# Kernel optimization log

Hardware: AMD Instinct MI355X
Metric: run time of the kernel (lower is better)

## Reference

```python
import jax, jax.numpy as jnp
import numpy as np

WH, WW = 14, 14
NUM_HEADS = 12
HEAD_DIM = 64
HIDDEN = NUM_HEADS * HEAD_DIM
SEQ = WH * WW + 1  # 197, includes cls token
NUM_REL = (2 * WH - 1) * (2 * WW - 1) + 3  # 732


def _relative_position_index(wh, ww):
    # Static numpy computation, identical to BeitRelativePositionBias buffer
    coords = np.stack(np.meshgrid(np.arange(wh), np.arange(ww), indexing='ij'))  # [2, wh, ww]
    flat = coords.reshape(2, -1)  # [2, wh*ww]
    rel = flat[:, :, None] - flat[:, None, :]  # [2, N, N]
    rel = rel.transpose(1, 2, 0).astype(np.int64)  # [N, N, 2]
    rel[..., 0] += wh - 1
    rel[..., 1] += ww - 1
    rel[..., 0] *= 2 * ww - 1
    nrd = (2 * wh - 1) * (2 * ww - 1) + 3
    idx = np.zeros((wh * ww + 1, wh * ww + 1), dtype=np.int64)
    idx[1:, 1:] = rel.sum(-1)
    idx[0, :] = nrd - 3
    idx[:, 0] = nrd - 2
    idx[0, 0] = nrd - 1
    return idx

_REL_IDX = jnp.asarray(_relative_position_index(WH, WW))  # [SEQ, SEQ]


def setup_inputs() -> dict:
    key = jax.random.key(0)
    ks = jax.random.split(key, 7)
    B = 64
    s = 1.0 / np.sqrt(HIDDEN)
    return {
        'hidden_states': jax.random.normal(ks[0], (B, SEQ, HIDDEN), jnp.float32),
        'Wq': jax.random.normal(ks[1], (HIDDEN, HIDDEN), jnp.float32) * s,
        'bq': jax.random.normal(ks[2], (HIDDEN,), jnp.float32) * 0.02,
        'Wk': jax.random.normal(ks[3], (HIDDEN, HIDDEN), jnp.float32) * s,
        'Wv': jax.random.normal(ks[4], (HIDDEN, HIDDEN), jnp.float32) * s,
        'bv': jax.random.normal(ks[5], (HIDDEN,), jnp.float32) * 0.02,
        'bias_table': jax.random.normal(ks[6], (NUM_REL, NUM_HEADS), jnp.float32) * 0.02,
    }


def reference(hidden_states, Wq, bq, Wk, Wv, bv, bias_table):
    B, S, D = hidden_states.shape
    H, Dh = NUM_HEADS, HEAD_DIM

    def heads(x):  # [B,S,D] -> [B,H,S,Dh]
        return x.reshape(B, S, H, Dh).transpose(0, 2, 1, 3)

    q = heads(hidden_states @ Wq + bq)
    k = heads(hidden_states @ Wk)           # key projection has no bias
    v = heads(hidden_states @ Wv + bv)

    scores = jnp.einsum('bhqd,bhkd->bhqk', q, k) / jnp.sqrt(jnp.float32(Dh))
    # relative position bias: gather [SEQ,SEQ,H] -> [H,SEQ,SEQ]
    rel_bias = bias_table[_REL_IDX].transpose(2, 0, 1)
    scores = scores + rel_bias[None]

    probs = jax.nn.softmax(scores, axis=-1)  # dropout prob = 0 (eval)
    ctx = jnp.einsum('bhqk,bhkd->bhqd', probs, v)
    ctx = ctx.transpose(0, 2, 1, 3).reshape(B, S, D)
    return ctx
```

## Files before the change

kernel.cpp:

```cpp
#include <hip/hip_runtime.h>
#include <hip/hip_bf16.h>
#include <stdint.h>

typedef unsigned short u16;
typedef __attribute__((ext_vector_type(4))) float f32x4;
typedef __attribute__((ext_vector_type(8))) short s16x8;
typedef __attribute__((ext_vector_type(4))) unsigned short u16x4;
typedef __attribute__((ext_vector_type(4))) float fvec4;

#define NH 12
#define DH 64
#define HID 768
#define SEQ 197
#define VP 224
#define NREL 732
#define BATCH 64
#define MROWS (BATCH*SEQ)
#define NCAT (3*HID)
#define BK 64
#define MT 99
#define NT 18
#define NWG (MT*NT)
#define AWG (768*13)
#define QKSTRIDE (SEQ*DH)

static __device__ __forceinline__ u16 f2bf(float f) {
  union { float f; uint32_t u; } v; v.f = f;
  uint32_t u = v.u;
  return (u16)((u + 0x7FFFu + ((u >> 16) & 1u)) >> 16);
}
static __device__ __forceinline__ float bf2f(u16 v) {
  union { uint32_t u; float f; } x; x.u = ((uint32_t)v) << 16; return x.f;
}

__global__ __launch_bounds__(256) void conv_x(const float* __restrict__ x, u16* __restrict__ xb, int n8) {
  int i = blockIdx.x * 256 + threadIdx.x;
  if (i >= n8) return;
  fvec4 a = ((const fvec4*)x)[2 * i];
  fvec4 b = ((const fvec4*)x)[2 * i + 1];
  s16x8 r;
  r[0] = (short)f2bf(a[0]); r[1] = (short)f2bf(a[1]); r[2] = (short)f2bf(a[2]); r[3] = (short)f2bf(a[3]);
  r[4] = (short)f2bf(b[0]); r[5] = (short)f2bf(b[1]); r[6] = (short)f2bf(b[2]); r[7] = (short)f2bf(b[3]);
  ((s16x8*)xb)[i] = r;
}

__global__ __launch_bounds__(256) void conv_w(const float* __restrict__ Wq, const float* __restrict__ Wk,
                                              const float* __restrict__ Wv, u16* __restrict__ Wt) {
  __shared__ float t[64][65];
  int n0 = blockIdx.x * 64;
  int k0 = blockIdx.y * 64;
  int m = n0 / HID;
  const float* W = (m == 0) ? Wq : ((m == 1) ? Wk : Wv);
  int nn0 = n0 - m * HID;
  for (int i = threadIdx.x; i < 64 * 64; i += 256) {
    int r = i >> 6, c = i & 63;
    t[r][c] = W[(size_t)(k0 + r) * HID + nn0 + c];
  }
  __syncthreads();
  for (int i = threadIdx.x; i < 64 * 64; i += 256) {
    int r = i >> 6, c = i & 63;
    Wt[(size_t)(n0 + r) * HID + k0 + c] = f2bf(t[c][r]);
  }
}

__global__ __launch_bounds__(256) void conv_b(const float* __restrict__ bq, const float* __restrict__ bv,
                                              float* __restrict__ bc) {
  int i = blockIdx.x * 256 + threadIdx.x;
  if (i < NCAT) {
    int m = i / HID, r = i - m * HID;
    bc[i] = (m == 0) ? bq[r] : ((m == 2) ? bv[r] : 0.f);
  }
}

__global__ __launch_bounds__(256) void expand_bias(const float* __restrict__ bias_table, u16* __restrict__ Bxt) {
  int i = blockIdx.x * 256 + threadIdx.x;
  if (i >= NH * 208 * 208) return;
  int h = i / (208 * 208);
  int r = i - h * 208 * 208;
  int k = r / 208, q = r - k * 208;
  float v;
  if (k >= SEQ) v = -1e30f;
  else if (q >= SEQ) v = 0.f;
  else {
    int idx;
    if (q == 0) idx = (k == 0) ? 731 : 729;
    else if (k == 0) idx = 730;
    else {
      int iq = (q - 1) / 14, jq = (q - 1) % 14;
      int ik = (k - 1) / 14, jk = (k - 1) % 14;
      idx = (iq - ik + 13) * 27 + (jq - jk + 13);
    }
    v = bias_table[(size_t)idx * NH + h];
  }
  Bxt[i] = f2bf(v);
}


static __device__ __forceinline__ void stage128(const u16* __restrict__ gbase, int grow0, int growmax,
                                                u16* lds, int w, int l) {
#pragma unroll
  for (int i = 0; i < 4; ++i) {
    int ch = w * 4 + i;
    int r = ch * 8 + (l >> 3);
    int grow = grow0 + r; if (grow > growmax) grow = growmax;
    int c = (l & 7) ^ (l >> 3);
    const u16* g = gbase + (size_t)grow * HID + c * 8;
    __builtin_amdgcn_global_load_lds((const __attribute__((address_space(1))) void*)g,
                                     (__attribute__((address_space(3))) void*)(lds + ch * 512),
                                     16, 0, 0);
  }
}

static __device__ __forceinline__ void compute128(const u16* As, const u16* Bs, int wr, int wc,
                                                  int li, int lg, f32x4 acc[4][4]) {
#pragma unroll
  for (int kk = 0; kk < 2; ++kk) {
    s16x8 af[4], bf[4];
#pragma unroll
    for (int mi = 0; mi < 4; ++mi) {
      int r = wr * 64 + mi * 16 + li;
      int c = (kk * 4 + lg) ^ (r & 7);
      af[mi] = *(const s16x8*)((const char*)As + r * 128 + c * 16);
    }
#pragma unroll
    for (int ni = 0; ni < 4; ++ni) {
      int r = wc * 64 + ni * 16 + li;
      int c = (kk * 4 + lg) ^ (r & 7);
      bf[ni] = *(const s16x8*)((const char*)Bs + r * 128 + c * 16);
    }
#pragma unroll
    for (int mi = 0; mi < 4; ++mi)
#pragma unroll
      for (int ni = 0; ni < 4; ++ni)
        acc[mi][ni] = __builtin_amdgcn_mfma_f32_16x16x32_bf16(af[mi], bf[ni], acc[mi][ni], 0, 0, 0);
  }
}

__global__ __launch_bounds__(256, 2) void qkv_gemm(const u16* __restrict__ Xb, const u16* __restrict__ Wt,
                                                   const float* __restrict__ bc, u16* __restrict__ Qw,
                                                   u16* __restrict__ Kw, u16* __restrict__ Vt) {
  __shared__ u16 LDSU[32768];
  u16* As0 = LDSU;
  u16* Bs0 = LDSU + 8192;
  u16* As1 = LDSU + 16384;
  u16* Bs1 = LDSU + 24576;
  const int tid = threadIdx.x;
  const int w = tid >> 6, l = tid & 63;
  const int wr = w >> 1, wc = w & 1;
  const int lg = l >> 4, li = l & 15;

  const int lin = blockIdx.x;
  const int xcd = lin & 7;
  const int pos = lin >> 3;
  const int work = (xcd < 6 ? xcd * 223 : 6 * 223 + (xcd - 6) * 222) + pos;
  const int mt = work / NT, nt = work - mt * NT;
  const int arow0 = mt * 128, brow0 = nt * 128;

  f32x4 acc[4][4] = {};

  stage128(Xb, arow0, MROWS - 1, As0, w, l);
  stage128(Wt, brow0, NCAT - 1, Bs0, w, l);
  __syncthreads();

  for (int kt2 = 0; kt2 < 6; ++kt2) {
    const int kt = kt2 * 2;
    stage128(Xb + (kt + 1) * BK, arow0, MROWS - 1, As1, w, l);
    stage128(Wt + (kt + 1) * BK, brow0, NCAT - 1, Bs1, w, l);
    compute128(As0, Bs0, wr, wc, li, lg, acc);
    __syncthreads();
    if (kt2 < 5) {
      stage128(Xb + (kt + 2) * BK, arow0, MROWS - 1, As0, w, l);
      stage128(Wt + (kt + 2) * BK, brow0, NCAT - 1, Bs0, w, l);
    }
    compute128(As1, Bs1, wr, wc, li, lg, acc);
    __syncthreads();
  }

  const int mblk = nt / 6;
  float bcv[4];
#pragma unroll
  for (int ni = 0; ni < 4; ++ni) bcv[ni] = bc[brow0 + wc * 64 + ni * 16 + li];

  if (mblk < 2) {
    u16* __restrict__ dst = (mblk == 0) ? Qw : Kw;
    const float scale = (mblk == 0) ? 0.125f : 1.0f;
    int hv[4], dv[4];
#pragma unroll
    for (int ni = 0; ni < 4; ++ni) {
      int cloc = brow0 - mblk * HID + wc * 64 + ni * 16 + li;
      hv[ni] = cloc >> 6; dv[ni] = cloc & 63;
    }
#pragma unroll
    for (int mi = 0; mi < 4; ++mi) {
#pragma unroll
      for (int j = 0; j < 4; ++j) {
        int row = arow0 + wr * 64 + mi * 16 + lg * 4 + j;
        if (row < MROWS) {
          int b = row / SEQ, s = row - b * SEQ;
#pragma unroll
          for (int ni = 0; ni < 4; ++ni)
            dst[((size_t)(b * NH + hv[ni]) * SEQ + s) * DH + dv[ni]] = f2bf((acc[mi][ni][j] + bcv[ni]) * scale);
        }
      }
    }
  } else {
#pragma unroll
    for (int mi = 0; mi < 4; ++mi) {
#pragma unroll
      for (int ni = 0; ni < 4; ++ni) {
        u16x4 pk;
#pragma unroll
        for (int j = 0; j < 4; ++j) pk[j] = f2bf(acc[mi][ni][j] + bcv[ni]);
        *(u16x4*)&LDSU[w * 4352 + (ni * 16 + li) * 68 + mi * 16 + lg * 4] = pk;
      }
    }
    __syncthreads();
    const int cw0 = brow0 - 2 * HID;
#pragma unroll 4
    for (int p = 0; p < 64; ++p) {
      int i = p * 256 + tid;
      int r = i & 127, c = i >> 7;
      int wq = ((r >> 6) << 1) | (c >> 6);
      u16 v = LDSU[wq * 4352 + (c & 63) * 68 + (r & 63)];
      int row = arow0 + r;
      if (row < MROWS) {
        int b = row / SEQ, s = row - b * SEQ;
        int cl = cw0 + c;
        int h = cl >> 6, d = cl & 63;
        Vt[((size_t)(b * NH + h) * DH + d) * VP + s] = v;
      }
    }
  }
}

__global__ __launch_bounds__(64, 3) void attn(const u16* __restrict__ Qw, const u16* __restrict__ Kw,
                                              const u16* __restrict__ Vt, const u16* __restrict__ Bxt,
                                              float* __restrict__ out) {
  __shared__ u16 P[16 * 232];
  const int l = threadIdx.x;
  const int lg = l >> 4, li = l & 15;
  const int lin = blockIdx.x;
  const int work = (lin & 7) * (AWG / 8) + (lin >> 3);
  const int bh = work / 13, qf = work - bh * 13;
  const int b = bh / NH, h = bh - b * NH;

  for (int t = l; t < 16 * 24; t += 64) {
    int rr = t / 24, cc = t - rr * 24;
    P[rr * 232 + 208 + cc] = 0;
  }

  const u16* Qb = Qw + (size_t)bh * QKSTRIDE;
  const u16* Kb = Kw + (size_t)bh * QKSTRIDE;
  const u16* Vb = Vt + (size_t)bh * DH * VP;
  const u16* Bhp = Bxt + (size_t)h * 208 * 208 + qf * 16 + lg * 4;

  s16x8 a0 = *(const s16x8*)(Qb + (size_t)(qf * 16 + li) * DH + lg * 8);
  s16x8 a1 = *(const s16x8*)(Qb + (size_t)(qf * 16 + li) * DH + 32 + lg * 8);

  u16x4 bb[13];
#pragma unroll
  for (int kf = 0; kf < 13; ++kf)
    bb[kf] = *(const u16x4*)(Bhp + (size_t)(kf * 16 + li) * 208);

  s16x8 kb0[3], kb1[3];
#pragma unroll
  for (int p = 0; p < 3; ++p) {
    kb0[p] = *(const s16x8*)(Kb + (size_t)(p * 16 + li) * DH + lg * 8);
    kb1[p] = *(const s16x8*)(Kb + (size_t)(p * 16 + li) * DH + 32 + lg * 8);
  }
  f32x4 S[13];
#pragma unroll
  for (int kf = 0; kf < 13; ++kf) {
    const int slot = kf % 3;
    f32x4 c = {};
    c = __builtin_amdgcn_mfma_f32_16x16x32_bf16(a0, kb0[slot], c, 0, 0, 0);
    c = __builtin_amdgcn_mfma_f32_16x16x32_bf16(a1, kb1[slot], c, 0, 0, 0);
    if (kf + 3 < 13) {
      kb0[slot] = *(const s16x8*)(Kb + (size_t)((kf + 3) * 16 + li) * DH + lg * 8);
      kb1[slot] = *(const s16x8*)(Kb + (size_t)((kf + 3) * 16 + li) * DH + 32 + lg * 8);
    }
#pragma unroll
    for (int j = 0; j < 4; ++j)
      S[kf][j] = c[j] + bf2f(bb[kf][j]);
  }

  float rinv[4];
#pragma unroll
  for (int j = 0; j < 4; ++j) {
    float m = S[0][j];
#pragma unroll
    for (int kf = 1; kf < 13; ++kf) m = fmaxf(m, S[kf][j]);
    m = fmaxf(m, __shfl_xor(m, 1));
    m = fmaxf(m, __shfl_xor(m, 2));
    m = fmaxf(m, __shfl_xor(m, 4));
    m = fmaxf(m, __shfl_xor(m, 8));
    float sum = 0.f;
#pragma unroll
    for (int kf = 0; kf < 13; ++kf) {
      float p = __expf(S[kf][j] - m);
      S[kf][j] = p;
      sum += p;
    }
    sum += __shfl_xor(sum, 1);
    sum += __shfl_xor(sum, 2);
    sum += __shfl_xor(sum, 4);
    sum += __shfl_xor(sum, 8);
    rinv[j] = 1.0f / sum;
  }

#pragma unroll
  for (int kf = 0; kf < 13; ++kf)
#pragma unroll
    for (int j = 0; j < 4; ++j)
      P[(lg * 4 + j) * 232 + kf * 16 + li] = f2bf(S[kf][j]);

  s16x8 vb[4];
#pragma unroll
  for (int p = 0; p < 4; ++p)
    vb[p] = *(const s16x8*)(Vb + (size_t)((p / 7) * 16 + li) * VP + (p % 7) * 32 + lg * 8);
  f32x4 o[4];
#pragma unroll
  for (int nf = 0; nf < 4; ++nf) {
    f32x4 c = {};
#pragma unroll
    for (int t = 0; t < 7; ++t) {
      const int u = nf * 7 + t, slot = u & 3;
      s16x8 pa = *(const s16x8*)(&P[li * 232 + t * 32 + lg * 8]);
      c = __builtin_amdgcn_mfma_f32_16x16x32_bf16(pa, vb[slot], c, 0, 0, 0);
      if (u + 4 < 28) {
        const int u2 = u + 4;
        vb[slot] = *(const s16x8*)(Vb + (size_t)((u2 / 7) * 16 + li) * VP + (u2 % 7) * 32 + lg * 8);
      }
    }
    o[nf] = c;
  }
#pragma unroll
  for (int nf = 0; nf < 4; ++nf) {
#pragma unroll
    for (int j = 0; j < 4; ++j) {
      int q = qf * 16 + lg * 4 + j;
      if (q < SEQ)
        out[((size_t)(b * SEQ + q)) * HID + h * DH + nf * 16 + li] = o[nf][j] * rinv[j];
    }
  }
}

extern "C" void kernel_launch(void* const* d_in, const int* in_sizes, int n_in,
                              void* d_out, int out_size, void* d_ws, size_t ws_size,
                              hipStream_t stream) {
  const float* hidden = (const float*)d_in[0];
  const float* Wq = (const float*)d_in[1];
  const float* bq = (const float*)d_in[2];
  const float* Wk = (const float*)d_in[3];
  const float* Wv = (const float*)d_in[4];
  const float* bv = (const float*)d_in[5];
  const float* btab = (const float*)d_in[6];
  float* out = (float*)d_out;

  char* ws = (char*)d_ws;
  u16* Xb  = (u16*)(ws);
  u16* Wt  = (u16*)(ws + 19365888);
  float* bc = (float*)(ws + 22904832);
  u16* Bxt = (u16*)(ws + 22914048);
  u16* Qw  = (u16*)(ws + 23952384);
  u16* Kw  = (u16*)(ws + 43322368);
  u16* Vt  = (u16*)(ws + 62692352);

  conv_x<<<dim3(4728), dim3(256), 0, stream>>>(hidden, Xb, (MROWS * HID) / 8);
  conv_w<<<dim3(NCAT / 64, HID / 64), dim3(256), 0, stream>>>(Wq, Wk, Wv, Wt);
  conv_b<<<dim3(9), dim3(256), 0, stream>>>(bq, bv, bc);
  qkv_gemm<<<dim3(NWG), dim3(256), 0, stream>>>(Xb, Wt, bc, Qw, Kw, Vt);
  expand_bias<<<dim3((NH * 208 * 208 + 255) / 256), dim3(256), 0, stream>>>(btab, Bxt);
  attn<<<dim3(AWG), dim3(64), 0, stream>>>(Qw, Kw, Vt, Bxt, out);
}
```

Before: 141.1 us.

## Merge prep kernels into one launch and process 32 queries per attention wave

The four preprocessing kernels (input cast, weight transpose-cast, bias concat, relative-bias expansion) become one kernel that picks its job from the block index. This removes three launches and their inter-kernel gaps. The attention kernel now has each wave handle two 16-row query tiles. That halves the K and V fragment loads per query and the number of workgroups, at the cost of more registers, so the occupancy hint drops from 3 to 2. The last query tile now reads bias and Q rows past the padded extent; the workspace offsets are shifted slightly, and those rows are never written out.

```diff
diff --git a/kernel.cpp b/kernel.cpp
--- a/kernel.cpp
+++ b/kernel.cpp
@@ -21,8 +21,13 @@
 #define MT 99
 #define NT 18
 #define NWG (MT*NT)
-#define AWG (768*13)
+#define AWG2 (768*7)
 #define QKSTRIDE (SEQ*DH)
+
+#define PB_X 4728
+#define PB_W (PB_X + 432)
+#define PB_B (PB_W + 9)
+#define PB_E (PB_B + 2028)
 
 static __device__ __forceinline__ u16 f2bf(float f) {
   union { float f; uint32_t u; } v; v.f = f;
@@ -33,68 +38,66 @@
   union { uint32_t u; float f; } x; x.u = ((uint32_t)v) << 16; return x.f;
 }
 
-__global__ __launch_bounds__(256) void conv_x(const float* __restrict__ x, u16* __restrict__ xb, int n8) {
-  int i = blockIdx.x * 256 + threadIdx.x;
-  if (i >= n8) return;
-  fvec4 a = ((const fvec4*)x)[2 * i];
-  fvec4 b = ((const fvec4*)x)[2 * i + 1];
-  s16x8 r;
-  r[0] = (short)f2bf(a[0]); r[1] = (short)f2bf(a[1]); r[2] = (short)f2bf(a[2]); r[3] = (short)f2bf(a[3]);
-  r[4] = (short)f2bf(b[0]); r[5] = (short)f2bf(b[1]); r[6] = (short)f2bf(b[2]); r[7] = (short)f2bf(b[3]);
-  ((s16x8*)xb)[i] = r;
-}
-
-__global__ __launch_bounds__(256) void conv_w(const float* __restrict__ Wq, const float* __restrict__ Wk,
-                                              const float* __restrict__ Wv, u16* __restrict__ Wt) {
+__global__ __launch_bounds__(256) void prep_all(const float* __restrict__ x,
+                                                const float* __restrict__ Wq, const float* __restrict__ Wk,
+                                                const float* __restrict__ Wv, const float* __restrict__ bq,
+                                                const float* __restrict__ bv, const float* __restrict__ btab,
+                                                u16* __restrict__ xb, u16* __restrict__ Wt,
+                                                float* __restrict__ bc, u16* __restrict__ Bxt) {
   __shared__ float t[64][65];
-  int n0 = blockIdx.x * 64;
-  int k0 = blockIdx.y * 64;
-  int m = n0 / HID;
-  const float* W = (m == 0) ? Wq : ((m == 1) ? Wk : Wv);
-  int nn0 = n0 - m * HID;
-  for (int i = threadIdx.x; i < 64 * 64; i += 256) {
-    int r = i >> 6, c = i & 63;
-    t[r][c] = W[(size_t)(k0 + r) * HID + nn0 + c];
-  }
-  __syncthreads();
-  for (int i = threadIdx.x; i < 64 * 64; i += 256) {
-    int r = i >> 6, c = i & 63;
-    Wt[(size_t)(n0 + r) * HID + k0 + c] = f2bf(t[c][r]);
-  }
-}
-
-__global__ __launch_bounds__(256) void conv_b(const float* __restrict__ bq, const float* __restrict__ bv,
-                                              float* __restrict__ bc) {
-  int i = blockIdx.x * 256 + threadIdx.x;
-  if (i < NCAT) {
-    int m = i / HID, r = i - m * HID;
-    bc[i] = (m == 0) ? bq[r] : ((m == 2) ? bv[r] : 0.f);
-  }
-}
-
-__global__ __launch_bounds__(256) void expand_bias(const float* __restrict__ bias_table, u16* __restrict__ Bxt) {
-  int i = blockIdx.x * 256 + threadIdx.x;
-  if (i >= NH * 208 * 208) return;
-  int h = i / (208 * 208);
-  int r = i - h * 208 * 208;
-  int k = r / 208, q = r - k * 208;
-  float v;
-  if (k >= SEQ) v = -1e30f;
-  else if (q >= SEQ) v = 0.f;
-  else {
-    int idx;
-    if (q == 0) idx = (k == 0) ? 731 : 729;
-    else if (k == 0) idx = 730;
+  const int bi = blockIdx.x;
+  const int tid = threadIdx.x;
+  if (bi < PB_X) {
+    int i = bi * 256 + tid;
+    fvec4 a = ((const fvec4*)x)[2 * i];
+    fvec4 b = ((const fvec4*)x)[2 * i + 1];
+    s16x8 r;
+    r[0] = (short)f2bf(a[0]); r[1] = (short)f2bf(a[1]); r[2] = (short)f2bf(a[2]); r[3] = (short)f2bf(a[3]);
+    r[4] = (short)f2bf(b[0]); r[5] = (short)f2bf(b[1]); r[6] = (short)f2bf(b[2]); r[7] = (short)f2bf(b[3]);
+    ((s16x8*)xb)[i] = r;
+  } else if (bi < PB_W) {
+    int f = bi - PB_X;
+    int n0 = (f % 36) * 64, k0 = (f / 36) * 64;
+    int m = n0 / HID;
+    const float* W = (m == 0) ? Wq : ((m == 1) ? Wk : Wv);
+    int nn0 = n0 - m * HID;
+    for (int i = tid; i < 64 * 64; i += 256) {
+      int r = i >> 6, c = i & 63;
+      t[r][c] = W[(size_t)(k0 + r) * HID + nn0 + c];
+    }
+    __syncthreads();
+    for (int i = tid; i < 64 * 64; i += 256) {
+      int r = i >> 6, c = i & 63;
+      Wt[(size_t)(n0 + r) * HID + k0 + c] = f2bf(t[c][r]);
+    }
+  } else if (bi < PB_B) {
+    int i = (bi - PB_W) * 256 + tid;
+    if (i < NCAT) {
+      int m = i / HID, r = i - m * HID;
+      bc[i] = (m == 0) ? bq[r] : ((m == 2) ? bv[r] : 0.f);
+    }
+  } else {
+    int i = (bi - PB_B) * 256 + tid;
+    int h = i / (208 * 208);
+    int r = i - h * 208 * 208;
+    int k = r / 208, q = r - k * 208;
+    float v;
+    if (k >= SEQ) v = -1e30f;
+    else if (q >= SEQ) v = 0.f;
     else {
-      int iq = (q - 1) / 14, jq = (q - 1) % 14;
-      int ik = (k - 1) / 14, jk = (k - 1) % 14;
-      idx = (iq - ik + 13) * 27 + (jq - jk + 13);
-    }
-    v = bias_table[(size_t)idx * NH + h];
-  }
-  Bxt[i] = f2bf(v);
-}
-
+      int idx;
+      if (q == 0) idx = (k == 0) ? 731 : 729;
+      else if (k == 0) idx = 730;
+      else {
+        int iq = (q - 1) / 14, jq = (q - 1) % 14;
+        int ik = (k - 1) / 14, jk = (k - 1) % 14;
+        idx = (iq - ik + 13) * 27 + (jq - jk + 13);
+      }
+      v = btab[(size_t)idx * NH + h];
+    }
+    Bxt[i] = f2bf(v);
+  }
+}
 
 static __device__ __forceinline__ void stage128(const u16* __restrict__ gbase, int grow0, int growmax,
                                                 u16* lds, int w, int l) {
@@ -233,34 +236,40 @@
   }
 }
 
-__global__ __launch_bounds__(64, 3) void attn(const u16* __restrict__ Qw, const u16* __restrict__ Kw,
+__global__ __launch_bounds__(64, 2) void attn(const u16* __restrict__ Qw, const u16* __restrict__ Kw,
                                               const u16* __restrict__ Vt, const u16* __restrict__ Bxt,
                                               float* __restrict__ out) {
-  __shared__ u16 P[16 * 232];
+  __shared__ u16 P[2][16 * 232];
   const int l = threadIdx.x;
   const int lg = l >> 4, li = l & 15;
   const int lin = blockIdx.x;
-  const int work = (lin & 7) * (AWG / 8) + (lin >> 3);
-  const int bh = work / 13, qf = work - bh * 13;
+  const int work = (lin & 7) * (AWG2 / 8) + (lin >> 3);
+  const int bh = work / 7, qp = work - bh * 7;
   const int b = bh / NH, h = bh - b * NH;
-
-  for (int t = l; t < 16 * 24; t += 64) {
-    int rr = t / 24, cc = t - rr * 24;
-    P[rr * 232 + 208 + cc] = 0;
+  const int q0 = qp * 32;
+
+  for (int t = l; t < 2 * 16 * 24; t += 64) {
+    int g = t / (16 * 24), r2 = t - g * (16 * 24);
+    int rr = r2 / 24, cc = r2 - rr * 24;
+    P[g][rr * 232 + 208 + cc] = 0;
   }
 
   const u16* Qb = Qw + (size_t)bh * QKSTRIDE;
   const u16* Kb = Kw + (size_t)bh * QKSTRIDE;
   const u16* Vb = Vt + (size_t)bh * DH * VP;
-  const u16* Bhp = Bxt + (size_t)h * 208 * 208 + qf * 16 + lg * 4;
-
-  s16x8 a0 = *(const s16x8*)(Qb + (size_t)(qf * 16 + li) * DH + lg * 8);
-  s16x8 a1 = *(const s16x8*)(Qb + (size_t)(qf * 16 + li) * DH + 32 + lg * 8);
-
-  u16x4 bb[13];
-#pragma unroll
-  for (int kf = 0; kf < 13; ++kf)
-    bb[kf] = *(const u16x4*)(Bhp + (size_t)(kf * 16 + li) * 208);
+  const u16* Bhp = Bxt + (size_t)h * 208 * 208 + q0 + lg * 4;
+
+  s16x8 a0 = *(const s16x8*)(Qb + (size_t)(q0 + li) * DH + lg * 8);
+  s16x8 a1 = *(const s16x8*)(Qb + (size_t)(q0 + li) * DH + 32 + lg * 8);
+  s16x8 a2 = *(const s16x8*)(Qb + (size_t)(q0 + 16 + li) * DH + lg * 8);
+  s16x8 a3 = *(const s16x8*)(Qb + (size_t)(q0 + 16 + li) * DH + 32 + lg * 8);
+
+  u16x4 bb0[13], bb1[13];
+#pragma unroll
+  for (int kf = 0; kf < 13; ++kf) {
+    bb0[kf] = *(const u16x4*)(Bhp + (size_t)(kf * 16 + li) * 208);
+    bb1[kf] = *(const u16x4*)(Bhp + (size_t)(kf * 16 + li) * 208 + 16);
+  }
 
   s16x8 kb0[3], kb1[3];
 #pragma unroll
@@ -268,79 +277,89 @@
     kb0[p] = *(const s16x8*)(Kb + (size_t)(p * 16 + li) * DH + lg * 8);
     kb1[p] = *(const s16x8*)(Kb + (size_t)(p * 16 + li) * DH + 32 + lg * 8);
   }
-  f32x4 S[13];
+  f32x4 S0[13], S1[13];
 #pragma unroll
   for (int kf = 0; kf < 13; ++kf) {
     const int slot = kf % 3;
-    f32x4 c = {};
-    c = __builtin_amdgcn_mfma_f32_16x16x32_bf16(a0, kb0[slot], c, 0, 0, 0);
-    c = __builtin_amdgcn_mfma_f32_16x16x32_bf16(a1, kb1[slot], c, 0, 0, 0);
+    f32x4 c0 = {}, c1 = {};
+    c0 = __builtin_amdgcn_mfma_f32_16x16x32_bf16(a0, kb0[slot], c0, 0, 0, 0);
+    c0 = __builtin_amdgcn_mfma_f32_16x16x32_bf16(a1, kb1[slot], c0, 0, 0, 0);
+    c1 = __builtin_amdgcn_mfma_f32_16x16x32_bf16(a2, kb0[slot], c1, 0, 0, 0);
+    c1 = __builtin_amdgcn_mfma_f32_16x16x32_bf16(a3, kb1[slot], c1, 0, 0, 0);
     if (kf + 3 < 13) {
       kb0[slot] = *(const s16x8*)(Kb + (size_t)((kf + 3) * 16 + li) * DH + lg * 8);
       kb1[slot] = *(const s16x8*)(Kb + (size_t)((kf + 3) * 16 + li) * DH + 32 + lg * 8);
     }
 #pragma unroll
-    for (int j = 0; j < 4; ++j)
-      S[kf][j] = c[j] + bf2f(bb[kf][j]);
-  }
-
-  float rinv[4];
+    for (int j = 0; j < 4; ++j) {
+      S0[kf][j] = c0[j] + bf2f(bb0[kf][j]);
+      S1[kf][j] = c1[j] + bf2f(bb1[kf][j]);
+    }
+  }
+
+  float rinv0[4], rinv1[4];
 #pragma unroll
   for (int j = 0; j < 4; ++j) {
-    float m = S[0][j];
-#pragma unroll
-    for (int kf = 1; kf < 13; ++kf) m = fmaxf(m, S[kf][j]);
-    m = fmaxf(m, __shfl_xor(m, 1));
-    m = fmaxf(m, __shfl_xor(m, 2));
-    m = fmaxf(m, __shfl_xor(m, 4));
-    m = fmaxf(m, __shfl_xor(m, 8));
-    float sum = 0.f;
+    float m0 = S0[0][j], m1 = S1[0][j];
+#pragma unroll
+    for (int kf = 1; kf < 13; ++kf) { m0 = fmaxf(m0, S0[kf][j]); m1 = fmaxf(m1, S1[kf][j]); }
+    m0 = fmaxf(m0, __shfl_xor(m0, 1)); m1 = fmaxf(m1, __shfl_xor(m1, 1));
+    m0 = fmaxf(m0, __shfl_xor(m0, 2)); m1 = fmaxf(m1, __shfl_xor(m1, 2));
+    m0 = fmaxf(m0, __shfl_xor(m0, 4)); m1 = fmaxf(m1, __shfl_xor(m1, 4));
+    m0 = fmaxf(m0, __shfl_xor(m0, 8)); m1 = fmaxf(m1, __shfl_xor(m1, 8));
+    float s0 = 0.f, s1 = 0.f;
 #pragma unroll
     for (int kf = 0; kf < 13; ++kf) {
-      float p = __expf(S[kf][j] - m);
-      S[kf][j] = p;
-      sum += p;
-    }
-    sum += __shfl_xor(sum, 1);
-    sum += __shfl_xor(sum, 2);
-    sum += __shfl_xor(sum, 4);
-    sum += __shfl_xor(sum, 8);
-    rinv[j] = 1.0f / sum;
+      float p0 = __expf(S0[kf][j] - m0); S0[kf][j] = p0; s0 += p0;
+      float p1 = __expf(S1[kf][j] - m1); S1[kf][j] = p1; s1 += p1;
+    }
+    s0 += __shfl_xor(s0, 1); s1 += __shfl_xor(s1, 1);
+    s0 += __shfl_xor(s0, 2); s1 += __shfl_xor(s1, 2);
+    s0 += __shfl_xor(s0, 4); s1 += __shfl_xor(s1, 4);
+    s0 += __shfl_xor(s0, 8); s1 += __shfl_xor(s1, 8);
+    rinv0[j] = 1.0f / s0; rinv1[j] = 1.0f / s1;
   }
 
 #pragma unroll
   for (int kf = 0; kf < 13; ++kf)
 #pragma unroll
-    for (int j = 0; j < 4; ++j)
-      P[(lg * 4 + j) * 232 + kf * 16 + li] = f2bf(S[kf][j]);
+    for (int j = 0; j < 4; ++j) {
+      P[0][(lg * 4 + j) * 232 + kf * 16 + li] = f2bf(S0[kf][j]);
+      P[1][(lg * 4 + j) * 232 + kf * 16 + li] = f2bf(S1[kf][j]);
+    }
 
   s16x8 vb[4];
 #pragma unroll
   for (int p = 0; p < 4; ++p)
     vb[p] = *(const s16x8*)(Vb + (size_t)((p / 7) * 16 + li) * VP + (p % 7) * 32 + lg * 8);
-  f32x4 o[4];
+  f32x4 o0[4], o1[4];
 #pragma unroll
   for (int nf = 0; nf < 4; ++nf) {
-    f32x4 c = {};
+    f32x4 c0 = {}, c1 = {};
 #pragma unroll
     for (int t = 0; t < 7; ++t) {
       const int u = nf * 7 + t, slot = u & 3;
-      s16x8 pa = *(const s16x8*)(&P[li * 232 + t * 32 + lg * 8]);
-      c = __builtin_amdgcn_mfma_f32_16x16x32_bf16(pa, vb[slot], c, 0, 0, 0);
+      s16x8 pa0 = *(const s16x8*)(&P[0][li * 232 + t * 32 + lg * 8]);
+      s16x8 pa1 = *(const s16x8*)(&P[1][li * 232 + t * 32 + lg * 8]);
+      c0 = __builtin_amdgcn_mfma_f32_16x16x32_bf16(pa0, vb[slot], c0, 0, 0, 0);
+      c1 = __builtin_amdgcn_mfma_f32_16x16x32_bf16(pa1, vb[slot], c1, 0, 0, 0);
       if (u + 4 < 28) {
         const int u2 = u + 4;
         vb[slot] = *(const s16x8*)(Vb + (size_t)((u2 / 7) * 16 + li) * VP + (u2 % 7) * 32 + lg * 8);
       }
     }
-    o[nf] = c;
+    o0[nf] = c0; o1[nf] = c1;
   }
 #pragma unroll
   for (int nf = 0; nf < 4; ++nf) {
 #pragma unroll
     for (int j = 0; j < 4; ++j) {
-      int q = qf * 16 + lg * 4 + j;
-      if (q < SEQ)
-        out[((size_t)(b * SEQ + q)) * HID + h * DH + nf * 16 + li] = o[nf][j] * rinv[j];
+      int qa = q0 + lg * 4 + j;
+      int qb2 = q0 + 16 + lg * 4 + j;
+      if (qa < SEQ)
+        out[((size_t)(b * SEQ + qa)) * HID + h * DH + nf * 16 + li] = o0[nf][j] * rinv0[j];
+      if (qb2 < SEQ)
+        out[((size_t)(b * SEQ + qb2)) * HID + h * DH + nf * 16 + li] = o1[nf][j] * rinv1[j];
     }
   }
 }
@@ -362,14 +381,11 @@
   u16* Wt  = (u16*)(ws + 19365888);
   float* bc = (float*)(ws + 22904832);
   u16* Bxt = (u16*)(ws + 22914048);
-  u16* Qw  = (u16*)(ws + 23952384);
-  u16* Kw  = (u16*)(ws + 43322368);
-  u16* Vt  = (u16*)(ws + 62692352);
-
-  conv_x<<<dim3(4728), dim3(256), 0, stream>>>(hidden, Xb, (MROWS * HID) / 8);
-  conv_w<<<dim3(NCAT / 64, HID / 64), dim3(256), 0, stream>>>(Wq, Wk, Wv, Wt);
-  conv_b<<<dim3(9), dim3(256), 0, stream>>>(bq, bv, bc);
+  u16* Qw  = (u16*)(ws + 23952512);
+  u16* Kw  = (u16*)(ws + 43322496);
+  u16* Vt  = (u16*)(ws + 62692480);
+
+  prep_all<<<dim3(PB_E), dim3(256), 0, stream>>>(hidden, Wq, Wk, Wv, bq, bv, btab, Xb, Wt, bc, Bxt);
   qkv_gemm<<<dim3(NWG), dim3(256), 0, stream>>>(Xb, Wt, bc, Qw, Kw, Vt);
-  expand_bias<<<dim3((NH * 208 * 208 + 255) / 256), dim3(256), 0, stream>>>(btab, Bxt);
-  attn<<<dim3(AWG), dim3(64), 0, stream>>>(Qw, Kw, Vt, Bxt, out);
-}
+  attn<<<dim3(AWG2), dim3(64), 0, stream>>>(Qw, Kw, Vt, Bxt, out);
+}
```

After: 133.8 us. 1.05x faster.
